# Kernel optimization log

Hardware: AMD Instinct MI355X
Metric: run time of the kernel (lower is better)

Reference implementation:

```python
import jax, jax.numpy as jnp
import numpy as np


def setup_inputs() -> dict:
    key = jax.random.key(0)
    ks = jax.random.split(key, 5)
    b, t, q_dim, kv_dim, h = 16, 128, 256, 64, 4
    c = t - 1
    q_x = jax.random.normal(ks[0], (b, t, q_dim), dtype=jnp.float32)
    kv_x = jax.random.normal(ks[1], (b, t, c, kv_dim), dtype=jnp.float32)
    # Linear weights stored as [in, out]; no biases (bias=False in torch module).
    sq = 1.0 / np.sqrt(q_dim)
    sk = 1.0 / np.sqrt(kv_dim)
    Wq = jax.random.uniform(ks[2], (q_dim, kv_dim * h), jnp.float32, -sq, sq)
    Wk = jax.random.uniform(ks[3], (kv_dim, kv_dim * h), jnp.float32, -sk, sk)
    Wv = jax.random.uniform(ks[4], (kv_dim, kv_dim * h), jnp.float32, -sk, sk)
    return {"q_x": q_x, "kv_x": kv_x, "Wq": Wq, "Wk": Wk, "Wv": Wv}


def reference(q_x, kv_x, Wq, Wk, Wv):
    b, t, c, k = kv_x.shape  # c = t - 1
    h = Wq.shape[1] // k
    # projections
    q = (q_x @ Wq).reshape(b, t, h, k)          # [b,t,h,k]
    keys = (kv_x @ Wk).reshape(b, t, c, h, k)   # [b,t,c,h,k]
    vals = (kv_x @ Wv).reshape(b, t, c, h, k)
    # per-token attention over the c-sized context
    scores = jnp.einsum('bthk,btchk->bthc', q, keys) / jnp.sqrt(jnp.float32(k))
    w = jax.nn.softmax(scores, axis=-1)          # softmax over context dim
    out = jnp.einsum('bthc,btchk->bthk', w, vals)
    return out.reshape(b, t, h * k)
```

## Files before the change

kernel.cpp:

```cpp
#include <hip/hip_runtime.h>
#include <math.h>

#define Bdim 16
#define Tdim 128
#define Cdim 127
#define Hdim 4
#define QD   256
#define HK   256
#define BT   (Bdim * Tdim)

#define DPP_XOR1        0xB1
#define DPP_XOR2        0x4E
#define DPP_HALF_MIRROR 0x141
#define DPP_MIRROR      0x140
template<int CTRL>
__device__ __forceinline__ float dpp_movf(float x) {
    return __int_as_float(__builtin_amdgcn_update_dpp(
        0, __float_as_int(x), CTRL, 0xF, 0xF, true));
}
__device__ __forceinline__ float quad_sum(float v) {
    v += dpp_movf<DPP_XOR1>(v);
    v += dpp_movf<DPP_XOR2>(v);
    return v;
}
__device__ __forceinline__ float rows_sum(float v) {
    v += dpp_movf<DPP_HALF_MIRROR>(v);
    v += dpp_movf<DPP_MIRROR>(v);
    v += __shfl_xor(v, 16, 64);
    v += __shfl_xor(v, 32, 64);
    return v;
}
__device__ __forceinline__ float wx_red(float v) {
    v += dpp_movf<DPP_XOR1>(v);
    v += dpp_movf<DPP_XOR2>(v);
    v += dpp_movf<DPP_HALF_MIRROR>(v);
    v += dpp_movf<DPP_MIRROR>(v);
    v += __shfl_xor(v, 16, 64);
    return v;
}

__global__ __launch_bounds__(256) void precompute_M(
        const float* __restrict__ Wq, const float* __restrict__ Wk,
        float* __restrict__ M) {
    int i = blockIdx.x;
    int tid = threadIdx.x;
    int h = tid >> 6, m = tid & 63;
    const float4* wq4 = (const float4*)(Wq + (size_t)i * HK + h * 64);
    const float4* wk4 = (const float4*)(Wk + (size_t)m * HK + h * 64);
    float4 q[16], k[16];
    #pragma unroll
    for (int j = 0; j < 16; ++j) q[j] = wq4[j];
    #pragma unroll
    for (int j = 0; j < 16; ++j) k[j] = wk4[j];
    float acc = 0.f;
    #pragma unroll
    for (int j = 0; j < 16; ++j)
        acc = fmaf(q[j].x, k[j].x, fmaf(q[j].y, k[j].y,
              fmaf(q[j].z, k[j].z, fmaf(q[j].w, k[j].w, acc))));
    M[(size_t)i * HK + tid] = acc;
}

template <int NS>
__global__ __launch_bounds__(256) void qk_gemm(
        const float* __restrict__ q_x,
        const float* __restrict__ M,
        float* __restrict__ part) {
    const int KLEN = 256 / NS;
    __shared__ __align__(16) float q_s[16][256 / NS];
    int RB = blockIdx.x;
    int S  = blockIdx.y;
    int tid = threadIdx.x;

    for (int f = tid; f < 16 * KLEN / 4; f += 256) {
        int r = f / (KLEN / 4), kq = f % (KLEN / 4);
        *(float4*)&q_s[r][kq*4] =
            *(const float4*)(q_x + (size_t)(RB*16 + r) * QD + S * KLEN + kq * 4);
    }
    __syncthreads();

    float acc[16];
    #pragma unroll
    for (int r = 0; r < 16; ++r) acc[r] = 0.f;

    #pragma unroll
    for (int kk = 0; kk < KLEN / 4; ++kk) {
        int k = S * KLEN + kk * 4;
        float m0 = M[(size_t)(k+0) * HK + tid];
        float m1 = M[(size_t)(k+1) * HK + tid];
        float m2 = M[(size_t)(k+2) * HK + tid];
        float m3 = M[(size_t)(k+3) * HK + tid];
        #pragma unroll
        for (int r = 0; r < 16; ++r) {
            float4 qv = *(const float4*)&q_s[r][kk*4];
            acc[r] = fmaf(qv.x, m0, fmaf(qv.y, m1, fmaf(qv.z, m2, fmaf(qv.w, m3, acc[r]))));
        }
    }
    float* dst = part + (size_t)S * (BT*HK) + (size_t)RB * 16 * HK + tid;
    #pragma unroll
    for (int r = 0; r < 16; ++r) dst[r * HK] = acc[r];
}

template <int NS>
__global__ __launch_bounds__(512, 6) void attn_main(
        const float* __restrict__ kv_x,
        const float* __restrict__ qk_p,
        const float* __restrict__ Wv,
        float* __restrict__ out) {
    __shared__ __align__(16) float4 sX4[128 * 16];
    __shared__ __align__(16) float qk_s[HK];
    __shared__ __align__(16) float4 e4[128];
    __shared__ __align__(16) float4 wx4[Hdim * 16];
    __shared__ __align__(16) float4 reds[8];

    int bt  = blockIdx.x;
    int tid = threadIdx.x;

    const float4* Xg = (const float4*)(kv_x + (size_t)bt * (Cdim * 64));
    #pragma unroll
    for (int it = 0; it < 4; ++it) {
        int l = tid + it * 512;
        if (l < Cdim * 16) {
            int c = l >> 4, p = l & 15;
            __builtin_amdgcn_global_load_lds(
                (const __attribute__((address_space(1))) void*)(Xg + (c << 4) + (p ^ (c & 7))),
                (__attribute__((address_space(3))) void*)(sX4 + l), 16, 0, 0);
        }
    }
    if (tid >= 256 && tid < 320)
        ((float*)sX4)[Cdim * 64 + (tid - 256)] = 0.f;
    if (tid < 256) {
        float q = 0.f;
        #pragma unroll
        for (int s = 0; s < NS; ++s)
            q += qk_p[(size_t)s * (BT*HK) + (size_t)bt * HK + tid];
        qk_s[tid] = q;
    }
    __syncthreads();

    int lane = tid & 63;
    int wave = tid >> 6;
    int c  = tid >> 2;
    int qp = tid & 3;
    int sw = c & 7;

    float e0, e1, e2, e3;
    {
        const float4* xrow = sX4 + c * 16;
        float4 x0 = xrow[(qp*4 + 0) ^ sw];
        float4 x1 = xrow[(qp*4 + 1) ^ sw];
        float4 x2 = xrow[(qp*4 + 2) ^ sw];
        float4 x3 = xrow[(qp*4 + 3) ^ sw];
        const float4* qk4 = (const float4*)qk_s;
        float a0 = 0.f, a1 = 0.f, a2 = 0.f, a3 = 0.f;
        #pragma unroll
        for (int i = 0; i < 4; ++i) {
            float4 xi = (i == 0) ? x0 : (i == 1) ? x1 : (i == 2) ? x2 : x3;
            float4 q0 = qk4[0*16 + qp*4 + i];
            float4 q1 = qk4[1*16 + qp*4 + i];
            float4 q2 = qk4[2*16 + qp*4 + i];
            float4 q3 = qk4[3*16 + qp*4 + i];
            a0 = fmaf(q0.x, xi.x, fmaf(q0.y, xi.y, fmaf(q0.z, xi.z, fmaf(q0.w, xi.w, a0))));
            a1 = fmaf(q1.x, xi.x, fmaf(q1.y, xi.y, fmaf(q1.z, xi.z, fmaf(q1.w, xi.w, a1))));
            a2 = fmaf(q2.x, xi.x, fmaf(q2.y, xi.y, fmaf(q2.z, xi.z, fmaf(q2.w, xi.w, a2))));
            a3 = fmaf(q3.x, xi.x, fmaf(q3.y, xi.y, fmaf(q3.z, xi.z, fmaf(q3.w, xi.w, a3))));
        }
        a0 = quad_sum(a0); a1 = quad_sum(a1); a2 = quad_sum(a2); a3 = quad_sum(a3);
        bool valid = (c < Cdim);
        e0 = valid ? __expf(a0 * 0.125f) : 0.f;
        e1 = valid ? __expf(a1 * 0.125f) : 0.f;
        e2 = valid ? __expf(a2 * 0.125f) : 0.f;
        e3 = valid ? __expf(a3 * 0.125f) : 0.f;
    }
    if (qp == 0) e4[c] = make_float4(e0, e1, e2, e3);
    float t0 = rows_sum(e0), t1 = rows_sum(e1), t2 = rows_sum(e2), t3 = rows_sum(e3);
    if (lane == 0) reds[wave] = make_float4(t0, t1, t2, t3);
    __syncthreads();

    {
        int jc = tid >> 5;
        int mq = (lane >> 3) & 3;
        int cs = lane & 7;
        float4 A0 = {0,0,0,0}, A1 = {0,0,0,0}, A2 = {0,0,0,0}, A3 = {0,0,0,0};
        #pragma unroll
        for (int mm = 0; mm < 4; ++mm) {
            int cc = cs + 8 * (mq * 4 + mm);
            float4 x4 = sX4[cc * 16 + (jc ^ cs)];
            float4 ee = e4[cc];
            A0.x = fmaf(ee.x, x4.x, A0.x); A0.y = fmaf(ee.x, x4.y, A0.y);
            A0.z = fmaf(ee.x, x4.z, A0.z); A0.w = fmaf(ee.x, x4.w, A0.w);
            A1.x = fmaf(ee.y, x4.x, A1.x); A1.y = fmaf(ee.y, x4.y, A1.y);
            A1.z = fmaf(ee.y, x4.z, A1.z); A1.w = fmaf(ee.y, x4.w, A1.w);
            A2.x = fmaf(ee.z, x4.x, A2.x); A2.y = fmaf(ee.z, x4.y, A2.y);
            A2.z = fmaf(ee.z, x4.z, A2.z); A2.w = fmaf(ee.z, x4.w, A2.w);
            A3.x = fmaf(ee.w, x4.x, A3.x); A3.y = fmaf(ee.w, x4.y, A3.y);
            A3.z = fmaf(ee.w, x4.z, A3.z); A3.w = fmaf(ee.w, x4.w, A3.w);
        }
        A0.x = wx_red(A0.x); A0.y = wx_red(A0.y); A0.z = wx_red(A0.z); A0.w = wx_red(A0.w);
        A1.x = wx_red(A1.x); A1.y = wx_red(A1.y); A1.z = wx_red(A1.z); A1.w = wx_red(A1.w);
        A2.x = wx_red(A2.x); A2.y = wx_red(A2.y); A2.z = wx_red(A2.z); A2.w = wx_red(A2.w);
        A3.x = wx_red(A3.x); A3.y = wx_red(A3.y); A3.z = wx_red(A3.z); A3.w = wx_red(A3.w);
        if ((lane & 31) == 0) {
            wx4[0 * 16 + jc] = A0;
            wx4[1 * 16 + jc] = A1;
            wx4[2 * 16 + jc] = A2;
            wx4[3 * 16 + jc] = A3;
        }
    }
    __syncthreads();

    if (tid < 256) {
        int hh = tid >> 6, k = tid & 63;
        float4 sums = reds[0];
        #pragma unroll
        for (int w = 1; w < 8; ++w) {
            float4 r = reds[w];
            sums.x += r.x; sums.y += r.y; sums.z += r.z; sums.w += r.w;
        }
        float denom = (hh == 0) ? sums.x : (hh == 1) ? sums.y
                    : (hh == 2) ? sums.z : sums.w;
        float inv = 1.f / denom;
        const float* wvcol = Wv + hh * 64 + k;
        float acc = 0.f;
        #pragma unroll 4
        for (int jc = 0; jc < 16; ++jc) {
            float4 w4 = wx4[hh * 16 + jc];
            acc = fmaf(w4.x, wvcol[(size_t)(jc*4+0) * HK],
                  fmaf(w4.y, wvcol[(size_t)(jc*4+1) * HK],
                  fmaf(w4.z, wvcol[(size_t)(jc*4+2) * HK],
                  fmaf(w4.w, wvcol[(size_t)(jc*4+3) * HK], acc))));
        }
        out[(size_t)bt * HK + tid] = acc * inv;
    }
}

extern "C" void kernel_launch(void* const* d_in, const int* in_sizes, int n_in,
                              void* d_out, int out_size, void* d_ws, size_t ws_size,
                              hipStream_t stream) {
    const float* q_x  = (const float*)d_in[0];
    const float* kv_x = (const float*)d_in[1];
    const float* Wq   = (const float*)d_in[2];
    const float* Wk   = (const float*)d_in[3];
    const float* Wv   = (const float*)d_in[4];
    float* out = (float*)d_out;

    float* M     = (float*)d_ws;
    float* parts = M + 256 * 256;

    size_t need8 = (size_t)(256*256 + 8 * BT*HK) * sizeof(float);
    int nsplit = (ws_size >= need8) ? 8 : 1;

    precompute_M<<<256, 256, 0, stream>>>(Wq, Wk, M);
    if (nsplit == 8) {
        qk_gemm<8><<<dim3(128, 8), 256, 0, stream>>>(q_x, M, parts);
        attn_main<8><<<BT, 512, 0, stream>>>(kv_x, parts, Wv, out);
    } else {
        qk_gemm<1><<<dim3(128, 1), 256, 0, stream>>>(q_x, M, parts);
        attn_main<1><<<BT, 512, 0, stream>>>(kv_x, parts, Wv, out);
    }
}
```

Before: 42.68 us.

## Fuse query-key projection into one kernel and process two tokens per attention block

The separate Wq·Wkᵀ precompute and the split-K qk GEMM are replaced by a single kernel. For each block of 4 rows it first computes q = q_x·Wq, then applies Wkᵀ per head. This drops one launch and the partial-sum buffers that attn_main previously had to reduce. attn_main now loops over two (b,t) tokens per block, halving its grid and reusing the block setup. The trade-off is fewer resident blocks to hide the kv_x load latency, and each qk_fused block re-reads the full Wq from cache.

```diff
diff --git a/kernel.cpp b/kernel.cpp
--- a/kernel.cpp
+++ b/kernel.cpp
@@ -8,6 +8,7 @@
 #define QD   256
 #define HK   256
 #define BT   (Bdim * Tdim)
+#define AITER 2
 
 #define DPP_XOR1        0xB1
 #define DPP_XOR2        0x4E
@@ -39,71 +40,62 @@
     return v;
 }
 
-__global__ __launch_bounds__(256) void precompute_M(
-        const float* __restrict__ Wq, const float* __restrict__ Wk,
-        float* __restrict__ M) {
-    int i = blockIdx.x;
+__global__ __launch_bounds__(256) void qk_fused(
+        const float* __restrict__ q_x,
+        const float* __restrict__ Wq,
+        const float* __restrict__ Wk,
+        float* __restrict__ qk) {
+    __shared__ __align__(16) float q_s[4][256];
+    __shared__ __align__(16) float p_s[4][4][68];
+    int RB = blockIdx.x;
     int tid = threadIdx.x;
+    {
+        int r = tid >> 6, kq = tid & 63;
+        *(float4*)&q_s[r][kq*4] =
+            *(const float4*)(q_x + (size_t)(RB*4 + r) * QD + kq * 4);
+    }
+    __syncthreads();
+
+    float acc[4] = {0.f, 0.f, 0.f, 0.f};
+    #pragma unroll 4
+    for (int i4 = 0; i4 < 64; ++i4) {
+        float w0 = Wq[(size_t)(4*i4+0) * HK + tid];
+        float w1 = Wq[(size_t)(4*i4+1) * HK + tid];
+        float w2 = Wq[(size_t)(4*i4+2) * HK + tid];
+        float w3 = Wq[(size_t)(4*i4+3) * HK + tid];
+        #pragma unroll
+        for (int r = 0; r < 4; ++r) {
+            float4 qv = *(const float4*)&q_s[r][i4*4];
+            acc[r] = fmaf(qv.x, w0, fmaf(qv.y, w1, fmaf(qv.z, w2, fmaf(qv.w, w3, acc[r]))));
+        }
+    }
     int h = tid >> 6, m = tid & 63;
-    const float4* wq4 = (const float4*)(Wq + (size_t)i * HK + h * 64);
+    #pragma unroll
+    for (int r = 0; r < 4; ++r) p_s[r][h][m] = acc[r];
+    __syncthreads();
+
     const float4* wk4 = (const float4*)(Wk + (size_t)m * HK + h * 64);
-    float4 q[16], k[16];
-    #pragma unroll
-    for (int j = 0; j < 16; ++j) q[j] = wq4[j];
-    #pragma unroll
-    for (int j = 0; j < 16; ++j) k[j] = wk4[j];
-    float acc = 0.f;
-    #pragma unroll
-    for (int j = 0; j < 16; ++j)
-        acc = fmaf(q[j].x, k[j].x, fmaf(q[j].y, k[j].y,
-              fmaf(q[j].z, k[j].z, fmaf(q[j].w, k[j].w, acc))));
-    M[(size_t)i * HK + tid] = acc;
-}
-
-template <int NS>
-__global__ __launch_bounds__(256) void qk_gemm(
-        const float* __restrict__ q_x,
-        const float* __restrict__ M,
-        float* __restrict__ part) {
-    const int KLEN = 256 / NS;
-    __shared__ __align__(16) float q_s[16][256 / NS];
-    int RB = blockIdx.x;
-    int S  = blockIdx.y;
-    int tid = threadIdx.x;
-
-    for (int f = tid; f < 16 * KLEN / 4; f += 256) {
-        int r = f / (KLEN / 4), kq = f % (KLEN / 4);
-        *(float4*)&q_s[r][kq*4] =
-            *(const float4*)(q_x + (size_t)(RB*16 + r) * QD + S * KLEN + kq * 4);
-    }
-    __syncthreads();
-
-    float acc[16];
-    #pragma unroll
-    for (int r = 0; r < 16; ++r) acc[r] = 0.f;
-
-    #pragma unroll
-    for (int kk = 0; kk < KLEN / 4; ++kk) {
-        int k = S * KLEN + kk * 4;
-        float m0 = M[(size_t)(k+0) * HK + tid];
-        float m1 = M[(size_t)(k+1) * HK + tid];
-        float m2 = M[(size_t)(k+2) * HK + tid];
-        float m3 = M[(size_t)(k+3) * HK + tid];
+    float4 wkr[16];
+    #pragma unroll
+    for (int j = 0; j < 16; ++j) wkr[j] = wk4[j];
+    float a2[4] = {0.f, 0.f, 0.f, 0.f};
+    #pragma unroll
+    for (int j4 = 0; j4 < 16; ++j4) {
         #pragma unroll
-        for (int r = 0; r < 16; ++r) {
-            float4 qv = *(const float4*)&q_s[r][kk*4];
-            acc[r] = fmaf(qv.x, m0, fmaf(qv.y, m1, fmaf(qv.z, m2, fmaf(qv.w, m3, acc[r]))));
-        }
-    }
-    float* dst = part + (size_t)S * (BT*HK) + (size_t)RB * 16 * HK + tid;
-    #pragma unroll
-    for (int r = 0; r < 16; ++r) dst[r * HK] = acc[r];
-}
-
-template <int NS>
+        for (int r = 0; r < 4; ++r) {
+            float4 pv = *(const float4*)&p_s[r][h][j4*4];
+            a2[r] = fmaf(pv.x, wkr[j4].x, fmaf(pv.y, wkr[j4].y,
+                    fmaf(pv.z, wkr[j4].z, fmaf(pv.w, wkr[j4].w, a2[r]))));
+        }
+    }
+    #pragma unroll
+    for (int r = 0; r < 4; ++r)
+        qk[(size_t)(RB*4 + r) * HK + tid] = a2[r];
+}
+
 __global__ __launch_bounds__(512, 6) void attn_main(
         const float* __restrict__ kv_x,
-        const float* __restrict__ qk_p,
+        const float* __restrict__ qk_g,
         const float* __restrict__ Wv,
         float* __restrict__ out) {
     __shared__ __align__(16) float4 sX4[128 * 16];
@@ -112,124 +104,121 @@
     __shared__ __align__(16) float4 wx4[Hdim * 16];
     __shared__ __align__(16) float4 reds[8];
 
-    int bt  = blockIdx.x;
     int tid = threadIdx.x;
-
-    const float4* Xg = (const float4*)(kv_x + (size_t)bt * (Cdim * 64));
-    #pragma unroll
-    for (int it = 0; it < 4; ++it) {
-        int l = tid + it * 512;
-        if (l < Cdim * 16) {
-            int c = l >> 4, p = l & 15;
-            __builtin_amdgcn_global_load_lds(
-                (const __attribute__((address_space(1))) void*)(Xg + (c << 4) + (p ^ (c & 7))),
-                (__attribute__((address_space(3))) void*)(sX4 + l), 16, 0, 0);
-        }
-    }
-    if (tid >= 256 && tid < 320)
-        ((float*)sX4)[Cdim * 64 + (tid - 256)] = 0.f;
-    if (tid < 256) {
-        float q = 0.f;
-        #pragma unroll
-        for (int s = 0; s < NS; ++s)
-            q += qk_p[(size_t)s * (BT*HK) + (size_t)bt * HK + tid];
-        qk_s[tid] = q;
-    }
-    __syncthreads();
-
     int lane = tid & 63;
     int wave = tid >> 6;
     int c  = tid >> 2;
     int qp = tid & 3;
     int sw = c & 7;
 
-    float e0, e1, e2, e3;
-    {
-        const float4* xrow = sX4 + c * 16;
-        float4 x0 = xrow[(qp*4 + 0) ^ sw];
-        float4 x1 = xrow[(qp*4 + 1) ^ sw];
-        float4 x2 = xrow[(qp*4 + 2) ^ sw];
-        float4 x3 = xrow[(qp*4 + 3) ^ sw];
-        const float4* qk4 = (const float4*)qk_s;
-        float a0 = 0.f, a1 = 0.f, a2 = 0.f, a3 = 0.f;
+    for (int it = 0; it < AITER; ++it) {
+        int bt = blockIdx.x * AITER + it;
+
+        const float4* Xg = (const float4*)(kv_x + (size_t)bt * (Cdim * 64));
         #pragma unroll
-        for (int i = 0; i < 4; ++i) {
-            float4 xi = (i == 0) ? x0 : (i == 1) ? x1 : (i == 2) ? x2 : x3;
-            float4 q0 = qk4[0*16 + qp*4 + i];
-            float4 q1 = qk4[1*16 + qp*4 + i];
-            float4 q2 = qk4[2*16 + qp*4 + i];
-            float4 q3 = qk4[3*16 + qp*4 + i];
-            a0 = fmaf(q0.x, xi.x, fmaf(q0.y, xi.y, fmaf(q0.z, xi.z, fmaf(q0.w, xi.w, a0))));
-            a1 = fmaf(q1.x, xi.x, fmaf(q1.y, xi.y, fmaf(q1.z, xi.z, fmaf(q1.w, xi.w, a1))));
-            a2 = fmaf(q2.x, xi.x, fmaf(q2.y, xi.y, fmaf(q2.z, xi.z, fmaf(q2.w, xi.w, a2))));
-            a3 = fmaf(q3.x, xi.x, fmaf(q3.y, xi.y, fmaf(q3.z, xi.z, fmaf(q3.w, xi.w, a3))));
-        }
-        a0 = quad_sum(a0); a1 = quad_sum(a1); a2 = quad_sum(a2); a3 = quad_sum(a3);
-        bool valid = (c < Cdim);
-        e0 = valid ? __expf(a0 * 0.125f) : 0.f;
-        e1 = valid ? __expf(a1 * 0.125f) : 0.f;
-        e2 = valid ? __expf(a2 * 0.125f) : 0.f;
-        e3 = valid ? __expf(a3 * 0.125f) : 0.f;
-    }
-    if (qp == 0) e4[c] = make_float4(e0, e1, e2, e3);
-    float t0 = rows_sum(e0), t1 = rows_sum(e1), t2 = rows_sum(e2), t3 = rows_sum(e3);
-    if (lane == 0) reds[wave] = make_float4(t0, t1, t2, t3);
-    __syncthreads();
-
-    {
-        int jc = tid >> 5;
-        int mq = (lane >> 3) & 3;
-        int cs = lane & 7;
-        float4 A0 = {0,0,0,0}, A1 = {0,0,0,0}, A2 = {0,0,0,0}, A3 = {0,0,0,0};
-        #pragma unroll
-        for (int mm = 0; mm < 4; ++mm) {
-            int cc = cs + 8 * (mq * 4 + mm);
-            float4 x4 = sX4[cc * 16 + (jc ^ cs)];
-            float4 ee = e4[cc];
-            A0.x = fmaf(ee.x, x4.x, A0.x); A0.y = fmaf(ee.x, x4.y, A0.y);
-            A0.z = fmaf(ee.x, x4.z, A0.z); A0.w = fmaf(ee.x, x4.w, A0.w);
-            A1.x = fmaf(ee.y, x4.x, A1.x); A1.y = fmaf(ee.y, x4.y, A1.y);
-            A1.z = fmaf(ee.y, x4.z, A1.z); A1.w = fmaf(ee.y, x4.w, A1.w);
-            A2.x = fmaf(ee.z, x4.x, A2.x); A2.y = fmaf(ee.z, x4.y, A2.y);
-            A2.z = fmaf(ee.z, x4.z, A2.z); A2.w = fmaf(ee.z, x4.w, A2.w);
-            A3.x = fmaf(ee.w, x4.x, A3.x); A3.y = fmaf(ee.w, x4.y, A3.y);
-            A3.z = fmaf(ee.w, x4.z, A3.z); A3.w = fmaf(ee.w, x4.w, A3.w);
-        }
-        A0.x = wx_red(A0.x); A0.y = wx_red(A0.y); A0.z = wx_red(A0.z); A0.w = wx_red(A0.w);
-        A1.x = wx_red(A1.x); A1.y = wx_red(A1.y); A1.z = wx_red(A1.z); A1.w = wx_red(A1.w);
-        A2.x = wx_red(A2.x); A2.y = wx_red(A2.y); A2.z = wx_red(A2.z); A2.w = wx_red(A2.w);
-        A3.x = wx_red(A3.x); A3.y = wx_red(A3.y); A3.z = wx_red(A3.z); A3.w = wx_red(A3.w);
-        if ((lane & 31) == 0) {
-            wx4[0 * 16 + jc] = A0;
-            wx4[1 * 16 + jc] = A1;
-            wx4[2 * 16 + jc] = A2;
-            wx4[3 * 16 + jc] = A3;
-        }
-    }
-    __syncthreads();
-
-    if (tid < 256) {
-        int hh = tid >> 6, k = tid & 63;
-        float4 sums = reds[0];
-        #pragma unroll
-        for (int w = 1; w < 8; ++w) {
-            float4 r = reds[w];
-            sums.x += r.x; sums.y += r.y; sums.z += r.z; sums.w += r.w;
-        }
-        float denom = (hh == 0) ? sums.x : (hh == 1) ? sums.y
-                    : (hh == 2) ? sums.z : sums.w;
-        float inv = 1.f / denom;
-        const float* wvcol = Wv + hh * 64 + k;
-        float acc = 0.f;
-        #pragma unroll 4
-        for (int jc = 0; jc < 16; ++jc) {
-            float4 w4 = wx4[hh * 16 + jc];
-            acc = fmaf(w4.x, wvcol[(size_t)(jc*4+0) * HK],
-                  fmaf(w4.y, wvcol[(size_t)(jc*4+1) * HK],
-                  fmaf(w4.z, wvcol[(size_t)(jc*4+2) * HK],
-                  fmaf(w4.w, wvcol[(size_t)(jc*4+3) * HK], acc))));
-        }
-        out[(size_t)bt * HK + tid] = acc * inv;
+        for (int s = 0; s < 4; ++s) {
+            int l = tid + s * 512;
+            if (l < Cdim * 16) {
+                int cc = l >> 4, p = l & 15;
+                __builtin_amdgcn_global_load_lds(
+                    (const __attribute__((address_space(1))) void*)(Xg + (cc << 4) + (p ^ (cc & 7))),
+                    (__attribute__((address_space(3))) void*)(sX4 + l), 16, 0, 0);
+            }
+        }
+        if (tid >= 256 && tid < 320)
+            ((float*)sX4)[Cdim * 64 + (tid - 256)] = 0.f;
+        if (tid < 256)
+            qk_s[tid] = qk_g[(size_t)bt * HK + tid];
+        __syncthreads();
+
+        float e0, e1, e2, e3;
+        {
+            const float4* xrow = sX4 + c * 16;
+            float4 x0 = xrow[(qp*4 + 0) ^ sw];
+            float4 x1 = xrow[(qp*4 + 1) ^ sw];
+            float4 x2 = xrow[(qp*4 + 2) ^ sw];
+            float4 x3 = xrow[(qp*4 + 3) ^ sw];
+            const float4* qk4 = (const float4*)qk_s;
+            float a0 = 0.f, a1 = 0.f, a2 = 0.f, a3 = 0.f;
+            #pragma unroll
+            for (int i = 0; i < 4; ++i) {
+                float4 xi = (i == 0) ? x0 : (i == 1) ? x1 : (i == 2) ? x2 : x3;
+                float4 q0 = qk4[0*16 + qp*4 + i];
+                float4 q1 = qk4[1*16 + qp*4 + i];
+                float4 q2 = qk4[2*16 + qp*4 + i];
+                float4 q3 = qk4[3*16 + qp*4 + i];
+                a0 = fmaf(q0.x, xi.x, fmaf(q0.y, xi.y, fmaf(q0.z, xi.z, fmaf(q0.w, xi.w, a0))));
+                a1 = fmaf(q1.x, xi.x, fmaf(q1.y, xi.y, fmaf(q1.z, xi.z, fmaf(q1.w, xi.w, a1))));
+                a2 = fmaf(q2.x, xi.x, fmaf(q2.y, xi.y, fmaf(q2.z, xi.z, fmaf(q2.w, xi.w, a2))));
+                a3 = fmaf(q3.x, xi.x, fmaf(q3.y, xi.y, fmaf(q3.z, xi.z, fmaf(q3.w, xi.w, a3))));
+            }
+            a0 = quad_sum(a0); a1 = quad_sum(a1); a2 = quad_sum(a2); a3 = quad_sum(a3);
+            bool valid = (c < Cdim);
+            e0 = valid ? __expf(a0 * 0.125f) : 0.f;
+            e1 = valid ? __expf(a1 * 0.125f) : 0.f;
+            e2 = valid ? __expf(a2 * 0.125f) : 0.f;
+            e3 = valid ? __expf(a3 * 0.125f) : 0.f;
+        }
+        if (qp == 0) e4[c] = make_float4(e0, e1, e2, e3);
+        float t0 = rows_sum(e0), t1 = rows_sum(e1), t2 = rows_sum(e2), t3 = rows_sum(e3);
+        if (lane == 0) reds[wave] = make_float4(t0, t1, t2, t3);
+        __syncthreads();
+
+        {
+            int jc = tid >> 5;
+            int mq = (lane >> 3) & 3;
+            int cs = lane & 7;
+            float4 A0 = {0,0,0,0}, A1 = {0,0,0,0}, A2 = {0,0,0,0}, A3 = {0,0,0,0};
+            #pragma unroll
+            for (int mm = 0; mm < 4; ++mm) {
+                int cc = cs + 8 * (mq * 4 + mm);
+                float4 x4 = sX4[cc * 16 + (jc ^ cs)];
+                float4 ee = e4[cc];
+                A0.x = fmaf(ee.x, x4.x, A0.x); A0.y = fmaf(ee.x, x4.y, A0.y);
+                A0.z = fmaf(ee.x, x4.z, A0.z); A0.w = fmaf(ee.x, x4.w, A0.w);
+                A1.x = fmaf(ee.y, x4.x, A1.x); A1.y = fmaf(ee.y, x4.y, A1.y);
+                A1.z = fmaf(ee.y, x4.z, A1.z); A1.w = fmaf(ee.y, x4.w, A1.w);
+                A2.x = fmaf(ee.z, x4.x, A2.x); A2.y = fmaf(ee.z, x4.y, A2.y);
+                A2.z = fmaf(ee.z, x4.z, A2.z); A2.w = fmaf(ee.z, x4.w, A2.w);
+                A3.x = fmaf(ee.w, x4.x, A3.x); A3.y = fmaf(ee.w, x4.y, A3.y);
+                A3.z = fmaf(ee.w, x4.z, A3.z); A3.w = fmaf(ee.w, x4.w, A3.w);
+            }
+            A0.x = wx_red(A0.x); A0.y = wx_red(A0.y); A0.z = wx_red(A0.z); A0.w = wx_red(A0.w);
+            A1.x = wx_red(A1.x); A1.y = wx_red(A1.y); A1.z = wx_red(A1.z); A1.w = wx_red(A1.w);
+            A2.x = wx_red(A2.x); A2.y = wx_red(A2.y); A2.z = wx_red(A2.z); A2.w = wx_red(A2.w);
+            A3.x = wx_red(A3.x); A3.y = wx_red(A3.y); A3.z = wx_red(A3.z); A3.w = wx_red(A3.w);
+            if ((lane & 31) == 0) {
+                wx4[0 * 16 + jc] = A0;
+                wx4[1 * 16 + jc] = A1;
+                wx4[2 * 16 + jc] = A2;
+                wx4[3 * 16 + jc] = A3;
+            }
+        }
+        __syncthreads();
+
+        if (tid < 256) {
+            int hh = tid >> 6, k = tid & 63;
+            float4 sums = reds[0];
+            #pragma unroll
+            for (int w = 1; w < 8; ++w) {
+                float4 r = reds[w];
+                sums.x += r.x; sums.y += r.y; sums.z += r.z; sums.w += r.w;
+            }
+            float denom = (hh == 0) ? sums.x : (hh == 1) ? sums.y
+                        : (hh == 2) ? sums.z : sums.w;
+            float inv = 1.f / denom;
+            const float* wvcol = Wv + hh * 64 + k;
+            float acc = 0.f;
+            #pragma unroll 4
+            for (int jc = 0; jc < 16; ++jc) {
+                float4 w4 = wx4[hh * 16 + jc];
+                acc = fmaf(w4.x, wvcol[(size_t)(jc*4+0) * HK],
+                      fmaf(w4.y, wvcol[(size_t)(jc*4+1) * HK],
+                      fmaf(w4.z, wvcol[(size_t)(jc*4+2) * HK],
+                      fmaf(w4.w, wvcol[(size_t)(jc*4+3) * HK], acc))));
+            }
+            out[(size_t)bt * HK + tid] = acc * inv;
+        }
     }
 }
 
@@ -243,18 +232,8 @@
     const float* Wv   = (const float*)d_in[4];
     float* out = (float*)d_out;
 
-    float* M     = (float*)d_ws;
-    float* parts = M + 256 * 256;
-
-    size_t need8 = (size_t)(256*256 + 8 * BT*HK) * sizeof(float);
-    int nsplit = (ws_size >= need8) ? 8 : 1;
-
-    precompute_M<<<256, 256, 0, stream>>>(Wq, Wk, M);
-    if (nsplit == 8) {
-        qk_gemm<8><<<dim3(128, 8), 256, 0, stream>>>(q_x, M, parts);
-        attn_main<8><<<BT, 512, 0, stream>>>(kv_x, parts, Wv, out);
-    } else {
-        qk_gemm<1><<<dim3(128, 1), 256, 0, stream>>>(q_x, M, parts);
-        attn_main<1><<<BT, 512, 0, stream>>>(kv_x, parts, Wv, out);
-    }
-}
+    float* qk = (float*)d_ws;
+
+    qk_fused<<<BT / 4, 256, 0, stream>>>(q_x, Wq, Wk, qk);
+    attn_main<<<BT / AITER, 512, 0, stream>>>(kv_x, qk, Wv, out);
+}
```

New measurement: 53.70 us. 25.8% more time.
